# Optimization experiments

Hardware: AMD Instinct MI355X
Metric: run time of the kernel (lower is better)

The kernel has to match this reference:

```python
import jax, jax.numpy as jnp
import numpy as np

EPS_COS = 1e-8   # torch cosine_similarity eps
EPS_DEN = 1e-6   # denominator eps in original loss
TEMP = 0.1


def setup_inputs() -> dict:
    key = jax.random.key(0)
    k1, _ = jax.random.split(key)
    N, D = 16384, 2048
    x = jax.random.normal(k1, (N, D), dtype=jnp.float32)
    pos_pair = jnp.arange(2, dtype=jnp.int64)  # (i, j) = (0, 1), i != j
    return {"x": x, "pos_pair": pos_pair}


def reference(x, pos_pair):
    # x: [N, D]; pos_pair: [2] int indices (i, j)
    i = pos_pair[0]
    j = pos_pair[1]
    xi = x[i]                                        # [D] anchor
    # cosine similarity of anchor against every row (single fused matvec)
    dots = x @ xi                                    # [N]
    norms = jnp.maximum(jnp.linalg.norm(x, axis=1), EPS_COS)   # [N]
    ni = jnp.maximum(jnp.linalg.norm(xi), EPS_COS)
    cos = dots / (norms * ni)                        # [N]
    e = jnp.exp(cos / TEMP)                          # [N]
    # denominator sums over all k != i (k == j included, as in original)
    mask = jnp.arange(x.shape[0]) != i
    denominator = jnp.sum(jnp.where(mask, e, 0.0))
    nominator = e[j]
    loss = -jnp.log(nominator / (denominator + EPS_DEN))
    return loss.reshape(1)  # original returns shape [1]
```

## Files before the change

### kernel.cpp

```cpp
#include <hip/hip_runtime.h>
#include <math.h>

#define D 2048
#define EPS_COS 1e-8f
#define EPS_DEN 1e-6f
#define INV_TEMP 10.0f
#define TPB 256
#define WPB (TPB / 64)
#define NBLOCKS 2048

__device__ __forceinline__ void get_ij(const int* __restrict__ p, int n,
                                       int& i, int& j) {
    int i32 = p[0], j32 = p[1];
    if (i32 >= 0 && i32 < n && j32 >= 0 && j32 < n && i32 != j32) {
        i = i32; j = j32; return;
    }
    const long long* p64 = (const long long*)p;
    i = (int)p64[0]; j = (int)p64[1];
}

__global__ __launch_bounds__(TPB)
void e_kernel(const float* __restrict__ x, const int* __restrict__ pos,
              float* __restrict__ e_out, int n) {
    int i, j;
    get_ij(pos, n, i, j);
    const int lane  = threadIdx.x & 63;
    const int wave  = threadIdx.x >> 6;
    const int gwave = blockIdx.x * WPB + wave;
    const int row0  = gwave * 2;
    if (row0 >= n) return;

    const float4* __restrict__ xi = (const float4*)(x + (size_t)i * D);
    float4 b[8];
#pragma unroll
    for (int w = 0; w < 8; ++w) b[w] = xi[lane + w * 64];

    float sqi = 0.f;
#pragma unroll
    for (int w = 0; w < 8; ++w)
        sqi = fmaf(b[w].x, b[w].x, fmaf(b[w].y, b[w].y,
              fmaf(b[w].z, b[w].z, fmaf(b[w].w, b[w].w, sqi))));
#pragma unroll
    for (int off = 32; off; off >>= 1) sqi += __shfl_down(sqi, off);
    const float ni = fmaxf(sqrtf(sqi), EPS_COS);

    const float4* __restrict__ r0 = (const float4*)(x + (size_t)row0 * D);
    const float4* __restrict__ r1 = (const float4*)(x + (size_t)(row0 + 1) * D);
    float4 a0[8], a1[8];
#pragma unroll
    for (int w = 0; w < 8; ++w) a0[w] = r0[lane + w * 64];
#pragma unroll
    for (int w = 0; w < 8; ++w) a1[w] = r1[lane + w * 64];

    float d0 = 0.f, s0 = 0.f, d1 = 0.f, s1 = 0.f;
#pragma unroll
    for (int w = 0; w < 8; ++w) {
        d0 = fmaf(a0[w].x, b[w].x, fmaf(a0[w].y, b[w].y,
             fmaf(a0[w].z, b[w].z, fmaf(a0[w].w, b[w].w, d0))));
        s0 = fmaf(a0[w].x, a0[w].x, fmaf(a0[w].y, a0[w].y,
             fmaf(a0[w].z, a0[w].z, fmaf(a0[w].w, a0[w].w, s0))));
        d1 = fmaf(a1[w].x, b[w].x, fmaf(a1[w].y, b[w].y,
             fmaf(a1[w].z, b[w].z, fmaf(a1[w].w, b[w].w, d1))));
        s1 = fmaf(a1[w].x, a1[w].x, fmaf(a1[w].y, a1[w].y,
             fmaf(a1[w].z, a1[w].z, fmaf(a1[w].w, a1[w].w, s1))));
    }
#pragma unroll
    for (int off = 32; off; off >>= 1) {
        d0 += __shfl_down(d0, off);
        s0 += __shfl_down(s0, off);
        d1 += __shfl_down(d1, off);
        s1 += __shfl_down(s1, off);
    }
    if (lane == 0) {
        float e0 = expf(INV_TEMP * d0 / (fmaxf(sqrtf(s0), EPS_COS) * ni));
        float e1 = expf(INV_TEMP * d1 / (fmaxf(sqrtf(s1), EPS_COS) * ni));
        e_out[row0]     = e0;
        e_out[row0 + 1] = e1;
    }
}

__global__ __launch_bounds__(1024)
void loss_kernel(const float* __restrict__ e, const int* __restrict__ pos,
                 float* __restrict__ out, int n) {
    int i, j;
    get_ij(pos, n, i, j);
    const int t = threadIdx.x;
    const float4* __restrict__ e4 = (const float4*)e;

    float s = 0.f;
    for (int k = t; k < n / 4; k += 1024) {
        float4 v = e4[k];
        s += (v.x + v.y) + (v.z + v.w);
    }
#pragma unroll
    for (int off = 32; off; off >>= 1) s += __shfl_down(s, off);

    __shared__ float ls[16];
    if ((t & 63) == 0) ls[t >> 6] = s;
    __syncthreads();

    if (t == 0) {
        float tot = 0.f;
#pragma unroll
        for (int w = 0; w < 16; ++w) tot += ls[w];
        float den = tot - e[i];
        out[0] = -logf(e[j] / (den + EPS_DEN));
    }
}

extern "C" void kernel_launch(void* const* d_in, const int* in_sizes, int n_in,
                              void* d_out, int out_size, void* d_ws, size_t ws_size,
                              hipStream_t stream) {
    const float* x   = (const float*)d_in[0];
    const int*   pos = (const int*)d_in[1];
    float*       out = (float*)d_out;
    float*       e   = (float*)d_ws;

    const int n = in_sizes[0] / D;

    e_kernel<<<NBLOCKS, TPB, 0, stream>>>(x, pos, e, n);
    loss_kernel<<<1, 1024, 0, stream>>>(e, pos, out, n);
}
```

Baseline: 191.1 us.

## Fuse exp and loss reduction into one kernel with atomic last-block finish

Merges the per-row exp kernel and the single-block reduction kernel into one kernel. Each block reduces its denominator and nominator contributions, atomically adds them into 64 spread slots, and the last block (found with an atomic counter) computes the final loss. This drops the intermediate e buffer and the second launch, but adds a memset launch, atomics and a fence-based completion protocol.

```diff
diff --git a/kernel.cpp b/kernel.cpp
--- a/kernel.cpp
+++ b/kernel.cpp
@@ -6,8 +6,8 @@
 #define EPS_DEN 1e-6f
 #define INV_TEMP 10.0f
 #define TPB 256
-#define WPB (TPB / 64)
-#define NBLOCKS 2048
+#define WPB 4
+#define NSLOT 64
 
 __device__ __forceinline__ void get_ij(const int* __restrict__ p, int n,
                                        int& i, int& j) {
@@ -20,15 +20,19 @@
 }
 
 __global__ __launch_bounds__(TPB)
-void e_kernel(const float* __restrict__ x, const int* __restrict__ pos,
-              float* __restrict__ e_out, int n) {
+void fused_kernel(const float* __restrict__ x, const int* __restrict__ pos,
+                  float* __restrict__ out, float* __restrict__ accf,
+                  unsigned* __restrict__ accu, int n, int nblocks) {
     int i, j;
     get_ij(pos, n, i, j);
     const int lane  = threadIdx.x & 63;
     const int wave  = threadIdx.x >> 6;
     const int gwave = blockIdx.x * WPB + wave;
     const int row0  = gwave * 2;
-    if (row0 >= n) return;
+    const bool v0 = (row0     < n);
+    const bool v1 = (row0 + 1 < n);
+    const int  r0 = v0 ? row0     : 0;
+    const int  r1 = v1 ? row0 + 1 : 0;
 
     const float4* __restrict__ xi = (const float4*)(x + (size_t)i * D);
     float4 b[8];
@@ -44,13 +48,13 @@
     for (int off = 32; off; off >>= 1) sqi += __shfl_down(sqi, off);
     const float ni = fmaxf(sqrtf(sqi), EPS_COS);
 
-    const float4* __restrict__ r0 = (const float4*)(x + (size_t)row0 * D);
-    const float4* __restrict__ r1 = (const float4*)(x + (size_t)(row0 + 1) * D);
+    const float4* __restrict__ p0 = (const float4*)(x + (size_t)r0 * D);
+    const float4* __restrict__ p1 = (const float4*)(x + (size_t)r1 * D);
     float4 a0[8], a1[8];
 #pragma unroll
-    for (int w = 0; w < 8; ++w) a0[w] = r0[lane + w * 64];
+    for (int w = 0; w < 8; ++w) a0[w] = p0[lane + w * 64];
 #pragma unroll
-    for (int w = 0; w < 8; ++w) a1[w] = r1[lane + w * 64];
+    for (int w = 0; w < 8; ++w) a1[w] = p1[lane + w * 64];
 
     float d0 = 0.f, s0 = 0.f, d1 = 0.f, s1 = 0.f;
 #pragma unroll
@@ -71,40 +75,36 @@
         d1 += __shfl_down(d1, off);
         s1 += __shfl_down(s1, off);
     }
+
+    __shared__ float s_den[WPB], s_ej[WPB];
     if (lane == 0) {
-        float e0 = expf(INV_TEMP * d0 / (fmaxf(sqrtf(s0), EPS_COS) * ni));
-        float e1 = expf(INV_TEMP * d1 / (fmaxf(sqrtf(s1), EPS_COS) * ni));
-        e_out[row0]     = e0;
-        e_out[row0 + 1] = e1;
+        float e0 = v0 ? expf(INV_TEMP * d0 / (fmaxf(sqrtf(s0), EPS_COS) * ni)) : 0.f;
+        float e1 = v1 ? expf(INV_TEMP * d1 / (fmaxf(sqrtf(s1), EPS_COS) * ni)) : 0.f;
+        float den = 0.f;
+        if (v0 && r0 != i) den += e0;
+        if (v1 && r1 != i) den += e1;
+        s_den[wave] = den;
+        s_ej[wave]  = (v0 && r0 == j) ? e0 : ((v1 && r1 == j) ? e1 : 0.f);
     }
-}
-
-__global__ __launch_bounds__(1024)
-void loss_kernel(const float* __restrict__ e, const int* __restrict__ pos,
-                 float* __restrict__ out, int n) {
-    int i, j;
-    get_ij(pos, n, i, j);
-    const int t = threadIdx.x;
-    const float4* __restrict__ e4 = (const float4*)e;
-
-    float s = 0.f;
-    for (int k = t; k < n / 4; k += 1024) {
-        float4 v = e4[k];
-        s += (v.x + v.y) + (v.z + v.w);
-    }
-#pragma unroll
-    for (int off = 32; off; off >>= 1) s += __shfl_down(s, off);
-
-    __shared__ float ls[16];
-    if ((t & 63) == 0) ls[t >> 6] = s;
     __syncthreads();
 
-    if (t == 0) {
-        float tot = 0.f;
+    if (threadIdx.x == 0) {
+        float bden = s_den[0] + s_den[1] + s_den[2] + s_den[3];
+        float bej  = s_ej[0]  + s_ej[1]  + s_ej[2]  + s_ej[3];
+        float r  = atomicAdd(&accf[blockIdx.x & (NSLOT - 1)], bden);
+        float r2 = (bej != 0.f) ? atomicAdd(&accf[NSLOT], bej) : 0.f;
+        unsigned inc = 1u
+            + ((__float_as_uint(r)  == 0x7F800001u) ? 1u : 0u)
+            + ((__float_as_uint(r2) == 0x7F800001u) ? 1u : 0u);
+        asm volatile("s_waitcnt vmcnt(0)" ::: "memory");
+        unsigned old = atomicAdd(accu, inc);
+        if (old == (unsigned)(nblocks - 1)) {
+            float den = 0.f;
 #pragma unroll
-        for (int w = 0; w < 16; ++w) tot += ls[w];
-        float den = tot - e[i];
-        out[0] = -logf(e[j] / (den + EPS_DEN));
+            for (int s = 0; s < NSLOT; ++s) den += atomicAdd(&accf[s], 0.f);
+            float nom = atomicAdd(&accf[NSLOT], 0.f);
+            out[0] = -logf(nom / (den + EPS_DEN));
+        }
     }
 }
 
@@ -114,10 +114,13 @@
     const float* x   = (const float*)d_in[0];
     const int*   pos = (const int*)d_in[1];
     float*       out = (float*)d_out;
-    float*       e   = (float*)d_ws;
+    float*       accf = (float*)d_ws;
+    unsigned*    accu = (unsigned*)d_ws + NSLOT + 1;
 
     const int n = in_sizes[0] / D;
+    const int rows_per_block = WPB * 2;
+    const int nblocks = (n + rows_per_block - 1) / rows_per_block;
 
-    e_kernel<<<NBLOCKS, TPB, 0, stream>>>(x, pos, e, n);
-    loss_kernel<<<1, 1024, 0, stream>>>(e, pos, out, n);
+    hipMemsetAsync(d_ws, 0, (NSLOT + 2) * sizeof(float), stream);
+    fused_kernel<<<nblocks, TPB, 0, stream>>>(x, pos, out, accf, accu, n, nblocks);
 }
```

New measurement: 215.3 us. 12.7% more time.
